# Optimization experiments

Hardware: AMD Instinct MI355X
Metric: run time of the kernel (lower is better)

The kernel has to match this reference:

```python
import jax, jax.numpy as jnp
import numpy as np

N, T, V, C, K, F = 64, 300, 25, 64, 3, 64
I = F // 4  # inter_filters = filters // 4


def setup_inputs() -> dict:
    key = jax.random.key(0)
    ks = jax.random.split(key, 8)
    x = jax.random.normal(ks[0], (N, T, V, C), jnp.float32)
    A = jax.random.uniform(ks[1], (K, V, V), jnp.float32)
    W = jax.random.normal(ks[2], (C, K * F), jnp.float32) * 0.05   # 1x1 conv weight
    b = jax.random.normal(ks[3], (K * F,), jnp.float32) * 0.05     # conv bias
    Wq = jax.random.normal(ks[4], (K, C, I), jnp.float32) * 0.05   # per-K embedding_q
    bq = jax.random.normal(ks[5], (K, I), jnp.float32) * 0.05
    Wk = jax.random.normal(ks[6], (K, C, I), jnp.float32) * 0.05   # per-K embedding_k
    bk = jax.random.normal(ks[7], (K, I), jnp.float32) * 0.05
    return {"x": x, "A": A, "W": W, "b": b, "Wq": Wq, "bq": bq, "Wk": Wk, "bk": bk}


def reference(x, A, W, b, Wq, bq, Wk, bk):
    # x: (N,T,V,C); A: (K,V,V)
    n, t, v, c = x.shape
    k = A.shape[0]
    f = W.shape[1] // k
    i = Wq.shape[-1]
    d = t * i

    # main 1x1 conv (t_kernel_size=1) -> (N,T,V,K*F) -> (N,T,V,K,F)
    h = (jnp.einsum('ntvc,cf->ntvf', x, W) + b).reshape(n, t, v, k, f)

    # per-K query/key embeddings, vectorized over K: (K,N,T,V,I)
    q = jnp.einsum('ntvc,kci->kntvi', x, Wq) + bq[:, None, None, None, :]
    kk = jnp.einsum('ntvc,kci->kntvi', x, Wk) + bk[:, None, None, None, :]

    # A_1: transpose to (K,N,V,T,I) -> (K,N,V,T*I); A_2: (K,N,T,I,V) -> (K,N,T*I,V)
    q2 = q.transpose(0, 1, 3, 2, 4).reshape(k, n, v, d)
    k2 = kk.transpose(0, 1, 2, 4, 3).reshape(k, n, d, v)

    scale = np.float32(1.0 / np.sqrt(d))
    att = jax.nn.softmax(jnp.einsum('knvd,kndw->knvw', q2, k2) * scale, axis=-1)
    A_adapt = A[:, None, :, :] + att  # (K,N,V,V)

    # aggregation: y[n,t,w,c] = sum_{v,k} h[n,t,v,k,c] * A_adapt[k,n,v,w]
    y = jnp.einsum('ntvkc,knvw->ntwc', h, A_adapt)
    return y
```

## Files before the change

kernel.cpp:

```cpp
#include <hip/hip_runtime.h>

#define DI __device__ __forceinline__

typedef float f32x4 __attribute__((ext_vector_type(4)));
typedef short s16x8 __attribute__((ext_vector_type(8)));

constexpr int N_ = 64, T_ = 300, V_ = 25, C_ = 64, K_ = 3, F_ = 64, I_ = 16;

DI short f2bf(float f) {
  union { float f; unsigned u; } v; v.f = f;
  unsigned r = (v.u + 0x7fffu + ((v.u >> 16) & 1u)) >> 16;
  return (short)r;
}

__global__ __launch_bounds__(256, 2) void k1_scores(
    const float* __restrict__ x,
    const float* __restrict__ Wq, const float* __restrict__ bq,
    const float* __restrict__ Wk, const float* __restrict__ bk,
    float* __restrict__ Spart, int nChunks)
{
  __shared__ __align__(16) short Xl[112 * 64];
  __shared__ __align__(16) short Wt[96 * 64];
  __shared__ __align__(16) short Pq[4 * 32 * 64];
  __shared__ __align__(16) short Pk[4 * 32 * 64];
  __shared__ float bcl[96];

  const int tid = threadIdx.x;
  const int lane = tid & 63;
  const int wid = tid >> 6;
  const int g = lane >> 4;
  const int lo = lane & 15;
  const int n = blockIdx.y;
  const int p = blockIdx.x;

  for (int idx = tid; idx < 96 * 64; idx += 256) {
    int j = idx >> 6, c = idx & 63;
    float v;
    if (j < 48) v = Wq[(j >> 4) * (C_ * I_) + c * I_ + (j & 15)];
    else { int j2 = j - 48; v = Wk[(j2 >> 4) * (C_ * I_) + c * I_ + (j2 & 15)]; }
    Wt[j * 64 + (c ^ ((j & 7) << 3))] = f2bf(v);
  }
  if (tid < 96) bcl[tid] = (tid < 48) ? bq[tid] : bk[tid - 48];

  f32x4 acc[3];
#pragma unroll
  for (int j = 0; j < 3; ++j) acc[j] = (f32x4){0.f, 0.f, 0.f, 0.f};

  for (int chunk = 0; chunk < nChunks; ++chunk) {
    const int t0row = (p * nChunks + chunk) * 100;

    {
      const float* xb = x + (size_t)n * (T_ * V_ * C_) + (size_t)t0row * C_;
      for (int idx = tid; idx < 112 * 64; idx += 256) {
        int row = idx >> 6, c = idx & 63;
        float v = (row < 100) ? xb[idx] : 0.f;
        Xl[row * 64 + (c ^ ((row & 7) << 3))] = f2bf(v);
      }
    }
    __syncthreads();

    for (int i = 0; i < 11; ++i) {
      int tile = wid + i * 4;
      if (tile >= 42) break;
      int m = tile / 6, nt = tile % 6;
      float binit = bcl[nt * 16 + lo];
      f32x4 pacc = { binit, binit, binit, binit };
#pragma unroll
      for (int ks = 0; ks < 2; ++ks) {
        int arow = m * 16 + lo;
        s16x8 a = *(const s16x8*)&Xl[arow * 64 + ((ks * 32 + g * 8) ^ ((arow & 7) << 3))];
        int brow = nt * 16 + lo;
        s16x8 b = *(const s16x8*)&Wt[brow * 64 + ((ks * 32 + g * 8) ^ ((brow & 7) << 3))];
        pacc = __builtin_amdgcn_mfma_f32_16x16x32_bf16(a, b, pacc, 0, 0, 0);
      }
#pragma unroll
      for (int r = 0; r < 4; ++r) {
        int row = m * 16 + g * 4 + r;
        if (row < 100) {
          int t = row / 25, v = row - t * 25;
          int j = nt * 16 + lo;
          short val = f2bf(pacc[r]);
          if (j < 48) Pq[(t * 32 + v) * 64 + (j ^ ((v & 7) << 3))] = val;
          else        Pk[(t * 32 + v) * 64 + ((j - 48) ^ ((v & 7) << 3))] = val;
        }
      }
    }
    __syncthreads();

#pragma unroll
    for (int j = 0; j < 3; ++j) {
      int combo = wid + j * 4;
      int k = combo >> 2, vt = (combo >> 1) & 1, wt = combo & 1;
#pragma unroll
      for (int ks = 0; ks < 2; ++ks) {
        int t = ks * 2 + (g >> 1);
        int ib = (g & 1) * 8;
        int v = vt * 16 + lo;
        s16x8 a = *(const s16x8*)&Pq[(t * 32 + v) * 64 + ((k * 16 + ib) ^ ((v & 7) << 3))];
        int w = wt * 16 + lo;
        s16x8 b = *(const s16x8*)&Pk[(t * 32 + w) * 64 + ((k * 16 + ib) ^ ((w & 7) << 3))];
        acc[j] = __builtin_amdgcn_mfma_f32_16x16x32_bf16(a, b, acc[j], 0, 0, 0);
      }
    }
  }

#pragma unroll
  for (int j = 0; j < 3; ++j) {
    int combo = wid + j * 4;
    int k = combo >> 2, vt = (combo >> 1) & 1, wt = combo & 1;
#pragma unroll
    for (int r = 0; r < 4; ++r) {
      int v = vt * 16 + g * 4 + r;
      int w = wt * 16 + lo;
      if (v < 25 && w < 25)
        Spart[((size_t)p * 192 + (k * 64 + n)) * 625 + v * 25 + w] = acc[j][r];
    }
  }
}

__global__ void k2_softmax(const float* __restrict__ Spart,
                           const float* __restrict__ A,
                           unsigned short* __restrict__ AadT, int G)
{
  __shared__ float Ss[625];
  int bx = blockIdx.x;
  int k = bx >> 6;
  int tid = threadIdx.x;
  unsigned short* outb = AadT + (size_t)bx * 1024;
  for (int idx = tid; idx < 1024; idx += 256) outb[idx] = 0;

  for (int cell = tid; cell < 625; cell += 256) {
    float s = 0.f;
    for (int pp = 0; pp < G; ++pp)
      s += Spart[((size_t)pp * 192 + bx) * 625 + cell];
    Ss[cell] = s;
  }
  __syncthreads();

  if (tid < 25) {
    int v = tid;
    const float scale = 0.014433756729740645f;
    float s[25];
    float mx = -1e30f;
#pragma unroll
    for (int w = 0; w < 25; ++w) { s[w] = Ss[v * 25 + w] * scale; mx = fmaxf(mx, s[w]); }
    float sum = 0.f;
#pragma unroll
    for (int w = 0; w < 25; ++w) { s[w] = __expf(s[w] - mx); sum += s[w]; }
    float inv = 1.f / sum;
#pragma unroll
    for (int w = 0; w < 25; ++w) {
      float aad = A[(k * 25 + v) * 25 + w] + s[w] * inv;
      outb[w * 32 + v] = (unsigned short)f2bf(aad);
    }
  }
}

__global__ __launch_bounds__(256, 2) void k3_main(
    const float* __restrict__ x,
    const float* __restrict__ W, const float* __restrict__ b,
    const unsigned short* __restrict__ AadT, float* __restrict__ y)
{
  __shared__ __align__(16) short Xl[80 * 64];
  __shared__ __align__(16) short Wt[192 * 64];
  __shared__ __align__(16) short Ht[192 * 96];
  __shared__ __align__(16) short Al[3 * 32 * 32];
  __shared__ float bl[192];

  const int tid = threadIdx.x;
  const int lane = tid & 63;
  const int wid = tid >> 6;
  const int g = lane >> 4;
  const int lo = lane & 15;
  const int n = blockIdx.y;
  const int t0 = blockIdx.x * 3;

  for (int idx = tid; idx < 192 * 64; idx += 256) {
    int c = idx / 192, j = idx % 192;
    Wt[j * 64 + (c ^ ((j & 7) << 3))] = f2bf(W[idx]);
  }
  if (tid < 192) bl[tid] = b[tid];

  for (int idx = tid; idx < 3 * 1024; idx += 256) {
    int kk = idx >> 10, rem = idx & 1023, w = rem >> 5, v = rem & 31;
    unsigned short val = AadT[(size_t)(kk * 64 + n) * 1024 + rem];
    Al[(kk * 32 + w) * 32 + (v ^ ((w & 3) << 3))] = (short)val;
  }

  for (int idx = tid; idx < 192 * 24; idx += 256) {
    int kc = idx / 24, rem = idx % 24, t = rem >> 3, vv = 24 + (rem & 7);
    Ht[kc * 96 + ((t * 32 + vv) ^ ((kc & 3) << 3))] = 0;
  }

  {
    const float* xb = x + (size_t)n * (T_ * V_ * C_) + (size_t)t0 * (V_ * C_);
    for (int idx = tid; idx < 80 * 64; idx += 256) {
      int row = idx >> 6, c = idx & 63;
      float v = (row < 75) ? xb[idx] : 0.f;
      Xl[row * 64 + (c ^ ((row & 7) << 3))] = f2bf(v);
    }
  }
  __syncthreads();

#pragma unroll
  for (int i = 0; i < 15; ++i) {
    int tile = wid + i * 4;
    int m = tile / 12, nt = tile % 12;
    float binit = bl[nt * 16 + lo];
    f32x4 acc = { binit, binit, binit, binit };
#pragma unroll
    for (int ks = 0; ks < 2; ++ks) {
      int arow = m * 16 + lo;
      s16x8 a = *(const s16x8*)&Xl[arow * 64 + ((ks * 32 + g * 8) ^ ((arow & 7) << 3))];
      int brow = nt * 16 + lo;
      s16x8 bb = *(const s16x8*)&Wt[brow * 64 + ((ks * 32 + g * 8) ^ ((brow & 7) << 3))];
      acc = __builtin_amdgcn_mfma_f32_16x16x32_bf16(a, bb, acc, 0, 0, 0);
    }
#pragma unroll
    for (int r = 0; r < 4; ++r) {
      int row = m * 16 + g * 4 + r;
      if (row < 75) {
        int t = row / 25, v = row - t * 25;
        int kc = nt * 16 + lo;
        Ht[kc * 96 + ((t * 32 + v) ^ ((kc & 3) << 3))] = f2bf(acc[r]);
      }
    }
  }
  __syncthreads();

#pragma unroll
  for (int i = 0; i < 6; ++i) {
    int job = wid + i * 4;
    int t = job >> 3, rem = job & 7, wt = rem >> 2, ct = rem & 3;
    f32x4 acc = { 0.f, 0.f, 0.f, 0.f };
#pragma unroll
    for (int k3 = 0; k3 < 3; ++k3) {
      int w = wt * 16 + lo;
      s16x8 a = *(const s16x8*)&Al[(k3 * 32 + w) * 32 + ((g * 8) ^ ((w & 3) << 3))];
      int kc = k3 * 64 + ct * 16 + lo;
      s16x8 bb = *(const s16x8*)&Ht[kc * 96 + ((t * 32 + g * 8) ^ ((kc & 3) << 3))];
      acc = __builtin_amdgcn_mfma_f32_16x16x32_bf16(a, bb, acc, 0, 0, 0);
    }
#pragma unroll
    for (int r = 0; r < 4; ++r) {
      int w = wt * 16 + g * 4 + r;
      if (w < 25)
        y[(((size_t)n * T_ + t0 + t) * V_ + w) * C_ + ct * 16 + lo] = acc[r];
    }
  }
}

extern "C" void kernel_launch(void* const* d_in, const int* in_sizes, int n_in,
                              void* d_out, int out_size, void* d_ws, size_t ws_size,
                              hipStream_t stream) {
  const float* x  = (const float*)d_in[0];
  const float* A  = (const float*)d_in[1];
  const float* W  = (const float*)d_in[2];
  const float* b  = (const float*)d_in[3];
  const float* Wq = (const float*)d_in[4];
  const float* bq = (const float*)d_in[5];
  const float* Wk = (const float*)d_in[6];
  const float* bk = (const float*)d_in[7];
  float* y = (float*)d_out;

  unsigned short* AadT = (unsigned short*)d_ws;
  float* Spart = (float*)((char*)d_ws + 512 * 1024);

  const size_t base = 512 * 1024;
  const size_t perG = (size_t)192 * 625 * sizeof(float);
  int G = 25;
  if (base + 25 * perG > ws_size) G = 15;
  if (base + 15 * perG > ws_size) G = 5;
  int nChunks = 75 / G;

  k1_scores<<<dim3(G, 64), 256, 0, stream>>>(x, Wq, bq, Wk, bk, Spart, nChunks);
  k2_softmax<<<dim3(192), 256, 0, stream>>>(Spart, A, AadT, G);
  k3_main<<<dim3(100, 64), 256, 0, stream>>>(x, W, b, AadT, y);
}
```

Before: 622.9 us.

## Pre-convert x to padded bf16 and rebuild score and main kernels around it

Adds a prep kernel that converts x, once per call, into a swizzled, padded bf16 buffer in workspace, along with the bf16 weight matrices. The score and main kernels then use direct global-to-LDS loads with double-buffered chunk prefetch, keep weight fragments in registers, and process K slices in a loop so the H tile in LDS is smaller and occupancy can rise. This removes repeated fp32 loading and bf16 conversion of x in both consumers. The cost is an extra kernel launch and a full write and read of the bf16 x copy. The old kernels are kept as a fallback when the workspace is too small.

Result: slower. 748.9 us (+20.2%).

```diff
diff --git a/kernel.cpp b/kernel.cpp
--- a/kernel.cpp
+++ b/kernel.cpp
@@ -13,7 +13,274 @@
   return (short)r;
 }
 
-__global__ __launch_bounds__(256, 2) void k1_scores(
+DI unsigned pk2bf(float a, float b) {
+  union { float f; unsigned u; } x, y; x.f = a; y.f = b;
+  return __builtin_amdgcn_perm(y.u + 0x8000u, x.u + 0x8000u, 0x07060302u);
+}
+
+DI void gload_lds16(const void* g, void* l) {
+  __builtin_amdgcn_global_load_lds(
+      (const __attribute__((address_space(1))) unsigned*)g,
+      (__attribute__((address_space(3))) unsigned*)l, 16, 0, 0);
+}
+
+
+__global__ __launch_bounds__(256) void k0_prep(
+    const float* __restrict__ x, const float* __restrict__ Wq,
+    const float* __restrict__ Wk, const float* __restrict__ W,
+    unsigned short* __restrict__ xbf, unsigned short* __restrict__ wqk,
+    unsigned short* __restrict__ wm)
+{
+  const int tid = threadIdx.x, lane = tid & 63, wid = tid >> 6;
+
+  if (blockIdx.x < 8) {
+    for (int idx = blockIdx.x * 256 + tid; idx < 96 * 64; idx += 2048) {
+      int j = idx >> 6, c = idx & 63;
+      float v = (j < 48) ? Wq[(j >> 4) * (C_ * I_) + c * I_ + (j & 15)]
+                         : Wk[((j - 48) >> 4) * (C_ * I_) + c * I_ + ((j - 48) & 15)];
+      wqk[idx] = (unsigned short)f2bf(v);
+    }
+    for (int idx = blockIdx.x * 256 + tid; idx < 192 * 64; idx += 2048) {
+      int kc = idx >> 6, c = idx & 63;
+      wm[idx] = (unsigned short)f2bf(W[c * 192 + kc]);
+    }
+  }
+
+  int row = blockIdx.x * 4 + wid;
+  if (row < N_ * T_) {
+    const float* xr = x + (size_t)row * (V_ * C_);
+    unsigned short* outr = xbf + (size_t)row * (32 * 64);
+#pragma unroll
+    for (int w = 0; w < 8; ++w) {
+      int o = lane * 4 + w * 256;
+      int v = o >> 6, cs = o & 63;
+      int c0 = cs ^ ((v & 7) << 3);
+      uint2 val; val.x = 0u; val.y = 0u;
+      if (v < 25) {
+        f32x4 f = *(const f32x4*)(xr + v * 64 + c0);
+        val.x = pk2bf(f[0], f[1]); val.y = pk2bf(f[2], f[3]);
+      }
+      *(uint2*)(outr + o) = val;
+    }
+  }
+}
+
+__global__ __launch_bounds__(256, 3) void k1_scores(
+    const unsigned short* __restrict__ xbf, const unsigned short* __restrict__ wqk,
+    const float* __restrict__ bq, const float* __restrict__ bk,
+    float* __restrict__ Spart, int nChunks)
+{
+  __shared__ __align__(16) unsigned short Xl[128 * 64];
+  __shared__ __align__(16) unsigned short P[128 * 104];
+
+  const int tid = threadIdx.x, lane = tid & 63, wid = tid >> 6;
+  const int g = lane >> 4, lo = lane & 15;
+  const int n = blockIdx.y, p = blockIdx.x;
+  const int c0 = p * nChunks;
+  const int c1 = (c0 + nChunks < 75) ? c0 + nChunks : 75;
+
+  s16x8 wf[12];
+#pragma unroll
+  for (int mj = 0; mj < 6; ++mj)
+#pragma unroll
+    for (int ks = 0; ks < 2; ++ks)
+      wf[mj * 2 + ks] = *(const s16x8*)(wqk + (mj * 16 + lo) * 64 + ks * 32 + g * 8);
+
+  f32x4 bias4[6];
+#pragma unroll
+  for (int mj = 0; mj < 6; ++mj) {
+    const float* bp = (mj < 3) ? (bq + mj * 16 + g * 4) : (bk + (mj - 3) * 16 + g * 4);
+    bias4[mj] = *(const f32x4*)bp;
+  }
+
+  f32x4 acc[3];
+#pragma unroll
+  for (int j = 0; j < 3; ++j) acc[j] = (f32x4){0.f, 0.f, 0.f, 0.f};
+
+  const size_t nbase = (size_t)n * T_ * 2048;
+  if (c0 < c1) {
+    const char* src = (const char*)(xbf + nbase + (size_t)c0 * 4 * 2048);
+#pragma unroll
+    for (int it = 0; it < 4; ++it)
+      gload_lds16(src + it * 4096 + wid * 1024 + lane * 16,
+                  (char*)Xl + it * 4096 + wid * 1024);
+  }
+  __syncthreads();
+
+  for (int ch = c0; ch < c1; ++ch) {
+#pragma unroll
+    for (int i = 0; i < 12; ++i) {
+      int tile = wid + i * 4;
+      int mj = tile >> 3, ntv = tile & 7;
+      f32x4 pa = bias4[mj];
+      int tv = ntv * 16 + lo;
+#pragma unroll
+      for (int ks = 0; ks < 2; ++ks) {
+        s16x8 bfrag = *(const s16x8*)&Xl[tv * 64 + ((ks * 32 + g * 8) ^ ((tv & 7) << 3))];
+        pa = __builtin_amdgcn_mfma_f32_16x16x32_bf16(wf[mj * 2 + ks], bfrag, pa, 0, 0, 0);
+      }
+      int jb = mj * 16 + g * 4;
+      uint2 w2; w2.x = pk2bf(pa[0], pa[1]); w2.y = pk2bf(pa[2], pa[3]);
+      *(uint2*)&P[tv * 104 + jb] = w2;
+    }
+    __syncthreads();
+
+    if (ch + 1 < c1) {
+      const char* src = (const char*)(xbf + nbase + (size_t)(ch + 1) * 4 * 2048);
+#pragma unroll
+      for (int it = 0; it < 4; ++it)
+        gload_lds16(src + it * 4096 + wid * 1024 + lane * 16,
+                    (char*)Xl + it * 4096 + wid * 1024);
+    }
+
+#pragma unroll
+    for (int j = 0; j < 3; ++j) {
+      int combo = wid + j * 4;
+      int k = combo >> 2, vt = (combo >> 1) & 1, wt = combo & 1;
+#pragma unroll
+      for (int ks = 0; ks < 2; ++ks) {
+        int t = ks * 2 + (g >> 1), ib = (g & 1) * 8;
+        int v = vt * 16 + lo, w = wt * 16 + lo;
+        s16x8 aq = *(const s16x8*)&P[(t * 32 + v) * 104 + k * 16 + ib];
+        s16x8 bk2 = *(const s16x8*)&P[(t * 32 + w) * 104 + 48 + k * 16 + ib];
+        acc[j] = __builtin_amdgcn_mfma_f32_16x16x32_bf16(aq, bk2, acc[j], 0, 0, 0);
+      }
+    }
+    __syncthreads();
+  }
+
+#pragma unroll
+  for (int j = 0; j < 3; ++j) {
+    int combo = wid + j * 4;
+    int k = combo >> 2, vt = (combo >> 1) & 1, wt = combo & 1;
+#pragma unroll
+    for (int r = 0; r < 4; ++r) {
+      int v = vt * 16 + g * 4 + r;
+      int w = wt * 16 + lo;
+      if (v < 25 && w < 25)
+        Spart[((size_t)p * 192 + (k * 64 + n)) * 625 + v * 25 + w] = acc[j][r];
+    }
+  }
+}
+
+__global__ void k2_softmax(const float* __restrict__ Spart,
+                           const float* __restrict__ A,
+                           unsigned short* __restrict__ aad, int G)
+{
+  __shared__ float Ss[625];
+  int bx = blockIdx.x, k = bx >> 6, tid = threadIdx.x;
+  unsigned short* outb = aad + (size_t)bx * 1280;
+  for (int idx = tid; idx < 640; idx += 256) ((unsigned*)outb)[idx] = 0u;
+  for (int cell = tid; cell < 625; cell += 256) {
+    float s = 0.f;
+    for (int pp = 0; pp < G; ++pp)
+      s += Spart[((size_t)pp * 192 + bx) * 625 + cell];
+    Ss[cell] = s;
+  }
+  __syncthreads();
+  if (tid < 25) {
+    int v = tid;
+    const float scale = 0.014433756729740645f;
+    float s[25];
+    float mx = -1e30f;
+#pragma unroll
+    for (int w = 0; w < 25; ++w) { s[w] = Ss[v * 25 + w] * scale; mx = fmaxf(mx, s[w]); }
+    float sum = 0.f;
+#pragma unroll
+    for (int w = 0; w < 25; ++w) { s[w] = __expf(s[w] - mx); sum += s[w]; }
+    float inv = 1.f / sum;
+#pragma unroll
+    for (int w = 0; w < 25; ++w) {
+      float aadv = A[(k * 25 + v) * 25 + w] + s[w] * inv;
+      outb[w * 40 + v] = (unsigned short)f2bf(aadv);
+    }
+  }
+}
+
+__global__ __launch_bounds__(256, 3) void k3_main(
+    const unsigned short* __restrict__ xbf, const unsigned short* __restrict__ wm,
+    const float* __restrict__ b_, const unsigned short* __restrict__ aad,
+    float* __restrict__ y)
+{
+  __shared__ __align__(16) unsigned short Xl[128 * 64];
+  __shared__ __align__(16) unsigned short Ht[64 * 136];
+  __shared__ __align__(16) unsigned short Al[3 * 32 * 40];
+
+  const int tid = threadIdx.x, lane = tid & 63, wid = tid >> 6;
+  const int g = lane >> 4, lo = lane & 15;
+  const int n = blockIdx.y, t0 = blockIdx.x * 4;
+
+  {
+    const char* src = (const char*)(xbf + ((size_t)n * T_ + t0) * 2048);
+#pragma unroll
+    for (int it = 0; it < 4; ++it)
+      gload_lds16(src + it * 4096 + wid * 1024 + lane * 16,
+                  (char*)Xl + it * 4096 + wid * 1024);
+  }
+  for (int idx = tid; idx < 480; idx += 256) {
+    int k = idx / 160, rem = idx - k * 160;
+    s16x8 v = *(const s16x8*)(aad + ((size_t)(k * 64 + n)) * 1280 + rem * 8);
+    *(s16x8*)&Al[k * 1280 + rem * 8] = v;
+  }
+  __syncthreads();
+
+  f32x4 acc[8];
+#pragma unroll
+  for (int i = 0; i < 8; ++i) acc[i] = (f32x4){0.f, 0.f, 0.f, 0.f};
+
+  for (int k = 0; k < 3; ++k) {
+    s16x8 wf[8];
+    float bz[4];
+#pragma unroll
+    for (int nt = 0; nt < 4; ++nt) {
+      bz[nt] = b_[k * 64 + nt * 16 + lo];
+#pragma unroll
+      for (int ks = 0; ks < 2; ++ks)
+        wf[nt * 2 + ks] = *(const s16x8*)(wm + (k * 64 + nt * 16 + lo) * 64 + ks * 32 + g * 8);
+    }
+
+#pragma unroll
+    for (int i = 0; i < 8; ++i) {
+      int tile = wid + i * 4;
+      int m = tile >> 2, nt = tile & 3;
+      f32x4 ha = (f32x4){bz[nt], bz[nt], bz[nt], bz[nt]};
+      int tv = m * 16 + lo;
+#pragma unroll
+      for (int ks = 0; ks < 2; ++ks) {
+        s16x8 af = *(const s16x8*)&Xl[tv * 64 + ((ks * 32 + g * 8) ^ ((tv & 7) << 3))];
+        ha = __builtin_amdgcn_mfma_f32_16x16x32_bf16(af, wf[nt * 2 + ks], ha, 0, 0, 0);
+      }
+      int kcl = nt * 16 + lo, tvb = m * 16 + g * 4;
+      uint2 w2; w2.x = pk2bf(ha[0], ha[1]); w2.y = pk2bf(ha[2], ha[3]);
+      *(uint2*)&Ht[kcl * 136 + tvb] = w2;
+    }
+    __syncthreads();
+
+#pragma unroll
+    for (int i = 0; i < 8; ++i) {
+      int job = wid + i * 4;
+      int t = job >> 3, rem = job & 7, wt = rem >> 2, ct = rem & 3;
+      s16x8 af = *(const s16x8*)&Al[(k * 32 + wt * 16 + lo) * 40 + g * 8];
+      s16x8 bf_ = *(const s16x8*)&Ht[(ct * 16 + lo) * 136 + t * 32 + g * 8];
+      acc[i] = __builtin_amdgcn_mfma_f32_16x16x32_bf16(af, bf_, acc[i], 0, 0, 0);
+    }
+    __syncthreads();
+  }
+
+#pragma unroll
+  for (int i = 0; i < 8; ++i) {
+    int job = wid + i * 4;
+    int t = job >> 3, rem = job & 7, wt = rem >> 2, ct = rem & 3;
+#pragma unroll
+    for (int r = 0; r < 4; ++r) {
+      int w = wt * 16 + g * 4 + r;
+      if (w < 25)
+        y[(((size_t)n * T_ + t0 + t) * V_ + w) * C_ + ct * 16 + lo] = acc[i][r];
+    }
+  }
+}
+
+__global__ __launch_bounds__(256, 2) void k1_fb(
     const float* __restrict__ x,
     const float* __restrict__ Wq, const float* __restrict__ bq,
     const float* __restrict__ Wk, const float* __restrict__ bk,
@@ -24,15 +291,9 @@
   __shared__ __align__(16) short Pq[4 * 32 * 64];
   __shared__ __align__(16) short Pk[4 * 32 * 64];
   __shared__ float bcl[96];
-
-  const int tid = threadIdx.x;
-  const int lane = tid & 63;
-  const int wid = tid >> 6;
-  const int g = lane >> 4;
-  const int lo = lane & 15;
-  const int n = blockIdx.y;
-  const int p = blockIdx.x;
-
+  const int tid = threadIdx.x, lane = tid & 63, wid = tid >> 6;
+  const int g = lane >> 4, lo = lane & 15;
+  const int n = blockIdx.y, p = blockIdx.x;
   for (int idx = tid; idx < 96 * 64; idx += 256) {
     int j = idx >> 6, c = idx & 63;
     float v;
@@ -41,14 +302,11 @@
     Wt[j * 64 + (c ^ ((j & 7) << 3))] = f2bf(v);
   }
   if (tid < 96) bcl[tid] = (tid < 48) ? bq[tid] : bk[tid - 48];
-
   f32x4 acc[3];
 #pragma unroll
   for (int j = 0; j < 3; ++j) acc[j] = (f32x4){0.f, 0.f, 0.f, 0.f};
-
   for (int chunk = 0; chunk < nChunks; ++chunk) {
     const int t0row = (p * nChunks + chunk) * 100;
-
     {
       const float* xb = x + (size_t)n * (T_ * V_ * C_) + (size_t)t0row * C_;
       for (int idx = tid; idx < 112 * 64; idx += 256) {
@@ -58,7 +316,6 @@
       }
     }
     __syncthreads();
-
     for (int i = 0; i < 11; ++i) {
       int tile = wid + i * 4;
       if (tile >= 42) break;
@@ -86,7 +343,6 @@
       }
     }
     __syncthreads();
-
 #pragma unroll
     for (int j = 0; j < 3; ++j) {
       int combo = wid + j * 4;
@@ -102,8 +358,8 @@
         acc[j] = __builtin_amdgcn_mfma_f32_16x16x32_bf16(a, b, acc[j], 0, 0, 0);
       }
     }
-  }
-
+    __syncthreads();
+  }
 #pragma unroll
   for (int j = 0; j < 3; ++j) {
     int combo = wid + j * 4;
@@ -118,25 +374,19 @@
   }
 }
 
-__global__ void k2_softmax(const float* __restrict__ Spart,
-                           const float* __restrict__ A,
-                           unsigned short* __restrict__ AadT, int G)
+__global__ void k2_fb(const float* __restrict__ Spart, const float* __restrict__ A,
+                      unsigned short* __restrict__ AadT, int G)
 {
   __shared__ float Ss[625];
-  int bx = blockIdx.x;
-  int k = bx >> 6;
-  int tid = threadIdx.x;
+  int bx = blockIdx.x, k = bx >> 6, tid = threadIdx.x;
   unsigned short* outb = AadT + (size_t)bx * 1024;
   for (int idx = tid; idx < 1024; idx += 256) outb[idx] = 0;
-
   for (int cell = tid; cell < 625; cell += 256) {
     float s = 0.f;
-    for (int pp = 0; pp < G; ++pp)
-      s += Spart[((size_t)pp * 192 + bx) * 625 + cell];
+    for (int pp = 0; pp < G; ++pp) s += Spart[((size_t)pp * 192 + bx) * 625 + cell];
     Ss[cell] = s;
   }
   __syncthreads();
-
   if (tid < 25) {
     int v = tid;
     const float scale = 0.014433756729740645f;
@@ -156,7 +406,7 @@
   }
 }
 
-__global__ __launch_bounds__(256, 2) void k3_main(
+__global__ __launch_bounds__(256, 2) void k3_fb(
     const float* __restrict__ x,
     const float* __restrict__ W, const float* __restrict__ b,
     const unsigned short* __restrict__ AadT, float* __restrict__ y)
@@ -166,32 +416,23 @@
   __shared__ __align__(16) short Ht[192 * 96];
   __shared__ __align__(16) short Al[3 * 32 * 32];
   __shared__ float bl[192];
-
-  const int tid = threadIdx.x;
-  const int lane = tid & 63;
-  const int wid = tid >> 6;
-  const int g = lane >> 4;
-  const int lo = lane & 15;
-  const int n = blockIdx.y;
-  const int t0 = blockIdx.x * 3;
-
+  const int tid = threadIdx.x, lane = tid & 63, wid = tid >> 6;
+  const int g = lane >> 4, lo = lane & 15;
+  const int n = blockIdx.y, t0 = blockIdx.x * 3;
   for (int idx = tid; idx < 192 * 64; idx += 256) {
     int c = idx / 192, j = idx % 192;
     Wt[j * 64 + (c ^ ((j & 7) << 3))] = f2bf(W[idx]);
   }
   if (tid < 192) bl[tid] = b[tid];
-
   for (int idx = tid; idx < 3 * 1024; idx += 256) {
     int kk = idx >> 10, rem = idx & 1023, w = rem >> 5, v = rem & 31;
     unsigned short val = AadT[(size_t)(kk * 64 + n) * 1024 + rem];
     Al[(kk * 32 + w) * 32 + (v ^ ((w & 3) << 3))] = (short)val;
   }
-
   for (int idx = tid; idx < 192 * 24; idx += 256) {
     int kc = idx / 24, rem = idx % 24, t = rem >> 3, vv = 24 + (rem & 7);
     Ht[kc * 96 + ((t * 32 + vv) ^ ((kc & 3) << 3))] = 0;
   }
-
   {
     const float* xb = x + (size_t)n * (T_ * V_ * C_) + (size_t)t0 * (V_ * C_);
     for (int idx = tid; idx < 80 * 64; idx += 256) {
@@ -201,7 +442,6 @@
     }
   }
   __syncthreads();
-
 #pragma unroll
   for (int i = 0; i < 15; ++i) {
     int tile = wid + i * 4;
@@ -227,7 +467,6 @@
     }
   }
   __syncthreads();
-
 #pragma unroll
   for (int i = 0; i < 6; ++i) {
     int job = wid + i * 4;
@@ -263,17 +502,39 @@
   const float* bk = (const float*)d_in[7];
   float* y = (float*)d_out;
 
-  unsigned short* AadT = (unsigned short*)d_ws;
-  float* Spart = (float*)((char*)d_ws + 512 * 1024);
-
-  const size_t base = 512 * 1024;
-  const size_t perG = (size_t)192 * 625 * sizeof(float);
-  int G = 25;
-  if (base + 25 * perG > ws_size) G = 15;
-  if (base + 15 * perG > ws_size) G = 5;
-  int nChunks = 75 / G;
-
-  k1_scores<<<dim3(G, 64), 256, 0, stream>>>(x, Wq, bq, Wk, bk, Spart, nChunks);
-  k2_softmax<<<dim3(192), 256, 0, stream>>>(Spart, A, AadT, G);
-  k3_main<<<dim3(100, 64), 256, 0, stream>>>(x, W, b, AadT, y);
-}
+  const size_t xbf_off = 0;
+  const size_t xbf_sz  = (size_t)N_ * T_ * 32 * 64 * 2;
+  const size_t wqk_off = xbf_off + xbf_sz;
+  const size_t wm_off  = wqk_off + 96 * 64 * 2;
+  const size_t aad_off = wm_off + 192 * 64 * 2;
+  const size_t sp_off  = aad_off + (size_t)192 * 32 * 40 * 2;
+  const size_t perG    = (size_t)192 * 625 * sizeof(float);
+
+  if (ws_size >= sp_off + perG) {
+    unsigned short* xbf = (unsigned short*)((char*)d_ws + xbf_off);
+    unsigned short* wqk = (unsigned short*)((char*)d_ws + wqk_off);
+    unsigned short* wm  = (unsigned short*)((char*)d_ws + wm_off);
+    unsigned short* aad = (unsigned short*)((char*)d_ws + aad_off);
+    float* Spart = (float*)((char*)d_ws + sp_off);
+
+    int G = (int)((ws_size - sp_off) / perG);
+    if (G > 12) G = 12;
+    int nChunks = (75 + G - 1) / G;
+
+    k0_prep<<<dim3(4800), 256, 0, stream>>>(x, Wq, Wk, W, xbf, wqk, wm);
+    k1_scores<<<dim3(G, 64), 256, 0, stream>>>(xbf, wqk, bq, bk, Spart, nChunks);
+    k2_softmax<<<dim3(192), 256, 0, stream>>>(Spart, A, aad, G);
+    k3_main<<<dim3(75, 64), 256, 0, stream>>>(xbf, wm, b, aad, y);
+  } else {
+    unsigned short* AadT = (unsigned short*)d_ws;
+    float* Spart = (float*)((char*)d_ws + 512 * 1024);
+    const size_t base = 512 * 1024;
+    int G = 25;
+    if (base + 25 * perG > ws_size) G = 15;
+    if (base + 15 * perG > ws_size) G = 5;
+    int nChunks = 75 / G;
+    k1_fb<<<dim3(G, 64), 256, 0, stream>>>(x, Wq, bq, Wk, bk, Spart, nChunks);
+    k2_fb<<<dim3(192), 256, 0, stream>>>(Spart, A, AadT, G);
+    k3_fb<<<dim3(100, 64), 256, 0, stream>>>(x, W, b, AadT, y);
+  }
+}
```
